# Performance work log

Measured on AMD Instinct MI355X. Metric: run time of the kernel, lower is better.

## Reference

```python
import jax, jax.numpy as jnp
import numpy as np

B, L, D_MODEL = 2, 1024, 512
N_LAYERS, D_STATE, D_CONV = 6, 16, 4
D_INNER = 2 * D_MODEL          # Mamba default expand=2
DT_RANK = (D_MODEL + 15) // 16  # ceil(d_model/16) = 32
EPS = 1.1920929e-07             # torch RMSNorm default eps (fp32 machine eps)


def rmsnorm(x, w):
    return x * jax.lax.rsqrt(jnp.mean(x * x, axis=-1, keepdims=True) + EPS) * w


def selective_scan(u, dt, A, Bm, Cm, Dv):
    # u, dt: (B,L,E); A: (E,N); Bm, Cm: (B,L,N); Dv: (E,)
    dA = jnp.exp(jnp.einsum('ble,en->blen', dt, A))    # discretized A (ZOH)
    dBu = jnp.einsum('ble,bln->blen', dt * u, Bm)      # discretized B * u (Euler)

    def step(h, inp):
        dA_t, dBu_t, C_t = inp
        h = dA_t * h + dBu_t                           # (B,E,N) state update
        y = jnp.einsum('ben,bn->be', h, C_t)
        return h, y

    h0 = jnp.zeros((u.shape[0], u.shape[2], A.shape[1]), u.dtype)
    _, ys = jax.lax.scan(step, h0,
                         (dA.transpose(1, 0, 2, 3), dBu.transpose(1, 0, 2, 3),
                          Cm.transpose(1, 0, 2)))
    return ys.transpose(1, 0, 2) + u * Dv


def mamba_block(x, p):
    xz = jnp.einsum('bld,ed->ble', x, p['in_proj_w'])  # (B,L,2E)
    xi, z = jnp.split(xz, 2, axis=-1)
    # causal depthwise conv1d (kernel D_CONV) + bias + SiLU
    xc = jnp.pad(xi.transpose(0, 2, 1), ((0, 0), (0, 0), (D_CONV - 1, 0)))
    xc = jax.lax.conv_general_dilated(xc, p['conv_w'][:, None, :], (1,), 'VALID',
                                      feature_group_count=D_INNER)
    xi = jax.nn.silu(xc.transpose(0, 2, 1) + p['conv_b'])
    dbc = jnp.einsum('ble,re->blr', xi, p['x_proj_w'])  # (B,L,R+2N)
    dt, Bm, Cm = jnp.split(dbc, [DT_RANK, DT_RANK + D_STATE], axis=-1)
    dt = jax.nn.softplus(jnp.einsum('blr,er->ble', dt, p['dt_w']) + p['dt_b'])
    y = selective_scan(xi, dt, -jnp.exp(p['A_log']), Bm, Cm, p['D'])
    y = y * jax.nn.silu(z)                              # gate branch
    return jnp.einsum('ble,de->bld', y, p['out_w'])


def setup_inputs() -> dict:
    key = jax.random.key(0)
    ks = jax.random.split(key, 8)
    s = 0.02
    return {
        'x': jax.random.normal(ks[0], (B, L, D_MODEL), jnp.float32),
        'position_embedding': jax.random.normal(ks[1], (B, L, D_MODEL), jnp.float32) * 0.02,
        'norm_w': jnp.ones((D_MODEL,), jnp.float32),
        'in_proj_w': jax.random.normal(ks[2], (N_LAYERS, 2 * D_INNER, D_MODEL), jnp.float32) * s,
        'conv_w': jax.random.normal(ks[3], (N_LAYERS, D_INNER, D_CONV), jnp.float32) * 0.2,
        'conv_b': jnp.zeros((N_LAYERS, D_INNER), jnp.float32),
        'x_proj_w': jax.random.normal(ks[4], (N_LAYERS, DT_RANK + 2 * D_STATE, D_INNER), jnp.float32) * s,
        'dt_w': jax.random.normal(ks[5], (N_LAYERS, D_INNER, DT_RANK), jnp.float32) * s,
        'dt_b': jnp.full((N_LAYERS, D_INNER), -4.6, jnp.float32),  # softplus(dt_b) ~ 0.01
        'A_log': jnp.broadcast_to(
            jnp.log(jnp.arange(1, D_STATE + 1, dtype=jnp.float32)),
            (N_LAYERS, D_INNER, D_STATE)) + jnp.zeros((N_LAYERS, D_INNER, D_STATE), jnp.float32),
        'D': jnp.ones((N_LAYERS, D_INNER), jnp.float32),
        'out_w': jax.random.normal(ks[6], (N_LAYERS, D_MODEL, D_INNER), jnp.float32) * s,
    }


def reference(x, position_embedding, norm_w, in_proj_w, conv_w, conv_b,
              x_proj_w, dt_w, dt_b, A_log, D, out_w):
    stacked = dict(in_proj_w=in_proj_w, conv_w=conv_w, conv_b=conv_b,
                   x_proj_w=x_proj_w, dt_w=dt_w, dt_b=dt_b,
                   A_log=A_log, D=D, out_w=out_w)

    def body(h, p):
        h = h + position_embedding          # added at the start of every layer
        h = mamba_block(rmsnorm(h, norm_w), p)  # NOTE: no residual, per source
        return h, None

    h, _ = jax.lax.scan(body, x, stacked)
    return h
```

## Files before the change

kernel.cpp:

```cpp
#include <hip/hip_runtime.h>
#include <hip/hip_bf16.h>


typedef __attribute__((ext_vector_type(8))) short bf16x8;
typedef __attribute__((ext_vector_type(4))) float f32x4;

__device__ __forceinline__ float bf2f(unsigned short u) {
    unsigned int x = ((unsigned int)u) << 16;
    return __builtin_bit_cast(float, x);
}
__device__ __forceinline__ unsigned short f2bf(float f) {
    __hip_bfloat16 h = __float2bfloat16(f);
    return __builtin_bit_cast(unsigned short, h);
}
__device__ __forceinline__ float ldin(const void* p, size_t i, int isbf) {
    return isbf ? bf2f(((const unsigned short*)p)[i]) : ((const float*)p)[i];
}
__device__ __forceinline__ float softplus_f(float x) {
    return (x > 20.f) ? x : log1pf(__expf(x));
}
__device__ __forceinline__ void split2(float x, unsigned short& h, unsigned short& l) {
    h = f2bf(x);
    l = f2bf(x - bf2f(h));
}

#define S1 (6*2048*512)
#define S2 (6*512*1024)
#define S3 (6*64*1024)
#define S4 (6*1024*32)
__global__ __launch_bounds__(256) void wsplit_all(
    const void* __restrict__ ipw, const void* __restrict__ ow,
    const void* __restrict__ xpw, const void* __restrict__ dtw,
    const void* __restrict__ Dw,
    unsigned short* __restrict__ h1, unsigned short* __restrict__ l1,
    unsigned short* __restrict__ h2, unsigned short* __restrict__ l2,
    unsigned short* __restrict__ h3, unsigned short* __restrict__ l3,
    unsigned short* __restrict__ h4, unsigned short* __restrict__ l4,
    int* __restrict__ flag)
{
    int g = blockIdx.x * 256 + threadIdx.x;
    const int isbf = (*(const unsigned int*)Dw == 0x3F800000u) ? 0 : 1;
    if (g == 0) *flag = isbf;
    const void* src; unsigned short *dh, *dl; int i;
    if (g < S1)                { src = ipw; dh = h1; dl = l1; i = g; }
    else if (g < S1+S2)        { src = ow;  dh = h2; dl = l2; i = g - S1; }
    else if (g < S1+S2+S3)     { src = xpw; dh = h3; dl = l3; i = g - S1 - S2; }
    else if (g < S1+S2+S3+S4)  { src = dtw; dh = h4; dl = l4; i = g - S1 - S2 - S3; }
    else return;
    unsigned short hh, ll;
    split2(ldin(src, i, isbf), hh, ll);
    dh[i] = hh; dl[i] = ll;
}

__global__ __launch_bounds__(256) void gemm128(
    const unsigned short* __restrict__ Ah, const unsigned short* __restrict__ Al,
    int lda,
    const unsigned short* __restrict__ Wh, const unsigned short* __restrict__ Wl,
    long woff,
    float* __restrict__ Cf, int N, int K)
{
    __shared__ __align__(16) unsigned short As[2][128][40];
    __shared__ __align__(16) unsigned short Ws[2][128][40];

    const int m0 = blockIdx.x * 128, n0 = blockIdx.y * 128;
    const int t = threadIdx.x, lane = t & 63, wave = t >> 6;
    const int wm = (wave & 1) * 64, wn = (wave >> 1) * 64;
    const int srow = t >> 1, scol = (t & 1) * 16;

    const unsigned short* ah = Ah + (size_t)(m0 + srow) * lda + scol;
    const unsigned short* al = Al + (size_t)(m0 + srow) * lda + scol;
    const unsigned short* wh = Wh + woff + (size_t)(n0 + srow) * K + scol;
    const unsigned short* wl = Wl + woff + (size_t)(n0 + srow) * K + scol;

    f32x4 acc[4][4] = {};
    const int fm = lane & 15, fk = (lane >> 4) * 8;

    for (int k0 = 0; k0 < K; k0 += 32) {
        __syncthreads();
        *(uint4*)(&As[0][srow][scol])     = *(const uint4*)(ah + k0);
        *(uint4*)(&As[0][srow][scol + 8]) = *(const uint4*)(ah + k0 + 8);
        *(uint4*)(&As[1][srow][scol])     = *(const uint4*)(al + k0);
        *(uint4*)(&As[1][srow][scol + 8]) = *(const uint4*)(al + k0 + 8);
        *(uint4*)(&Ws[0][srow][scol])     = *(const uint4*)(wh + k0);
        *(uint4*)(&Ws[0][srow][scol + 8]) = *(const uint4*)(wh + k0 + 8);
        *(uint4*)(&Ws[1][srow][scol])     = *(const uint4*)(wl + k0);
        *(uint4*)(&Ws[1][srow][scol + 8]) = *(const uint4*)(wl + k0 + 8);
        __syncthreads();

        bf16x8 a_h[4], a_l[4], w_h[4], w_l[4];
#pragma unroll
        for (int i = 0; i < 4; ++i) {
            a_h[i] = *(const bf16x8*)(&As[0][wm + i * 16 + fm][fk]);
            a_l[i] = *(const bf16x8*)(&As[1][wm + i * 16 + fm][fk]);
            w_h[i] = *(const bf16x8*)(&Ws[0][wn + i * 16 + fm][fk]);
            w_l[i] = *(const bf16x8*)(&Ws[1][wn + i * 16 + fm][fk]);
        }
#pragma unroll
        for (int mi = 0; mi < 4; ++mi)
#pragma unroll
            for (int ni = 0; ni < 4; ++ni) {
                acc[mi][ni] = __builtin_amdgcn_mfma_f32_16x16x32_bf16(
                    a_h[mi], w_h[ni], acc[mi][ni], 0, 0, 0);
                acc[mi][ni] = __builtin_amdgcn_mfma_f32_16x16x32_bf16(
                    a_h[mi], w_l[ni], acc[mi][ni], 0, 0, 0);
                acc[mi][ni] = __builtin_amdgcn_mfma_f32_16x16x32_bf16(
                    a_l[mi], w_h[ni], acc[mi][ni], 0, 0, 0);
            }
    }

    const int col = lane & 15, rb = (lane >> 4) * 4;
#pragma unroll
    for (int mi = 0; mi < 4; ++mi)
#pragma unroll
        for (int ni = 0; ni < 4; ++ni)
#pragma unroll
            for (int r = 0; r < 4; ++r) {
                int gm = m0 + wm + mi * 16 + rb + r;
                int gn = n0 + wn + ni * 16 + col;
                Cf[(size_t)gm * N + gn] = acc[mi][ni][r];
            }
}

template <int ACT>
__global__ __launch_bounds__(256) void gemm_hl(
    const unsigned short* __restrict__ Ah, const unsigned short* __restrict__ Al,
    int lda,
    const unsigned short* __restrict__ Wh, const unsigned short* __restrict__ Wl,
    long woff,
    float* __restrict__ Cf, long zstride,
    const void* __restrict__ bias, long boff, const int* __restrict__ flag,
    int N, int K, int Kc)
{
    const int isbf = *flag;
    __shared__ __align__(16) unsigned short As[2][64][40];
    __shared__ __align__(16) unsigned short Ws[2][64][40];

    const int m0 = blockIdx.x * 64, n0 = blockIdx.y * 64;
    const int kb = blockIdx.z * Kc;
    const int t = threadIdx.x;
    const int lane = t & 63, wave = t >> 6;
    const int wm = (wave & 1) * 32, wn = (wave >> 1) * 32;
    const int srow = t >> 2, scol = (t & 3) * 8;

    const unsigned short* ah = Ah + (size_t)(m0 + srow) * lda + scol;
    const unsigned short* al = Al + (size_t)(m0 + srow) * lda + scol;
    const unsigned short* wh = Wh + woff + (size_t)(n0 + srow) * K + scol;
    const unsigned short* wl = Wl + woff + (size_t)(n0 + srow) * K + scol;

    f32x4 acc[2][2] = {};

    for (int k0 = kb; k0 < kb + Kc; k0 += 32) {
        __syncthreads();
        *(uint4*)(&As[0][srow][scol]) = *(const uint4*)(ah + k0);
        *(uint4*)(&As[1][srow][scol]) = *(const uint4*)(al + k0);
        *(uint4*)(&Ws[0][srow][scol]) = *(const uint4*)(wh + k0);
        *(uint4*)(&Ws[1][srow][scol]) = *(const uint4*)(wl + k0);
        __syncthreads();

        const int fm = lane & 15, fk = (lane >> 4) * 8;
        bf16x8 a0h = *(const bf16x8*)(&As[0][wm + fm][fk]);
        bf16x8 a1h = *(const bf16x8*)(&As[0][wm + 16 + fm][fk]);
        bf16x8 w0h = *(const bf16x8*)(&Ws[0][wn + fm][fk]);
        bf16x8 w1h = *(const bf16x8*)(&Ws[0][wn + 16 + fm][fk]);
        bf16x8 a0l = *(const bf16x8*)(&As[1][wm + fm][fk]);
        bf16x8 a1l = *(const bf16x8*)(&As[1][wm + 16 + fm][fk]);
        bf16x8 w0l = *(const bf16x8*)(&Ws[1][wn + fm][fk]);
        bf16x8 w1l = *(const bf16x8*)(&Ws[1][wn + 16 + fm][fk]);

        acc[0][0] = __builtin_amdgcn_mfma_f32_16x16x32_bf16(a0h, w0h, acc[0][0], 0, 0, 0);
        acc[0][1] = __builtin_amdgcn_mfma_f32_16x16x32_bf16(a0h, w1h, acc[0][1], 0, 0, 0);
        acc[1][0] = __builtin_amdgcn_mfma_f32_16x16x32_bf16(a1h, w0h, acc[1][0], 0, 0, 0);
        acc[1][1] = __builtin_amdgcn_mfma_f32_16x16x32_bf16(a1h, w1h, acc[1][1], 0, 0, 0);
        acc[0][0] = __builtin_amdgcn_mfma_f32_16x16x32_bf16(a0h, w0l, acc[0][0], 0, 0, 0);
        acc[0][1] = __builtin_amdgcn_mfma_f32_16x16x32_bf16(a0h, w1l, acc[0][1], 0, 0, 0);
        acc[1][0] = __builtin_amdgcn_mfma_f32_16x16x32_bf16(a1h, w0l, acc[1][0], 0, 0, 0);
        acc[1][1] = __builtin_amdgcn_mfma_f32_16x16x32_bf16(a1h, w1l, acc[1][1], 0, 0, 0);
        acc[0][0] = __builtin_amdgcn_mfma_f32_16x16x32_bf16(a0l, w0h, acc[0][0], 0, 0, 0);
        acc[0][1] = __builtin_amdgcn_mfma_f32_16x16x32_bf16(a0l, w1h, acc[0][1], 0, 0, 0);
        acc[1][0] = __builtin_amdgcn_mfma_f32_16x16x32_bf16(a1l, w0h, acc[1][0], 0, 0, 0);
        acc[1][1] = __builtin_amdgcn_mfma_f32_16x16x32_bf16(a1l, w1h, acc[1][1], 0, 0, 0);
    }

    float* Cp = Cf + (size_t)blockIdx.z * zstride;
    const int col = lane & 15, rb = (lane >> 4) * 4;
#pragma unroll
    for (int mi = 0; mi < 2; ++mi)
#pragma unroll
        for (int ni = 0; ni < 2; ++ni)
#pragma unroll
            for (int r = 0; r < 4; ++r) {
                int gm = m0 + wm + mi * 16 + rb + r;
                int gn = n0 + wn + ni * 16 + col;
                float v = acc[mi][ni][r];
                if (bias) v += ldin(bias, boff + gn, isbf);
                if (ACT == 1) v = softplus_f(v);
                Cp[(size_t)gm * N + gn] = v;
            }
}

__global__ __launch_bounds__(256) void xp_reduce(
    const float* __restrict__ Pxp, float* __restrict__ dbc,
    unsigned short* __restrict__ dth, unsigned short* __restrict__ dtl)
{
    int g = blockIdx.x * 256 + threadIdx.x;
    float s = 0.f;
#pragma unroll
    for (int z = 0; z < 8; ++z) s += Pxp[(size_t)z * 131072 + g];
    dbc[g] = s;
    int n = g & 63, t = g >> 6;
    if (n < 32) {
        unsigned short hh, ll;
        split2(s, hh, ll);
        dth[t * 32 + n] = hh; dtl[t * 32 + n] = ll;
    }
}

__global__ __launch_bounds__(256) void rmsnorm_k(
    const void* __restrict__ hsrc, int hdyn, const void* __restrict__ pos,
    const void* __restrict__ nw, const int* __restrict__ flag,
    unsigned short* __restrict__ xnh, unsigned short* __restrict__ xnl)
{
    const int isbf = *flag;
    const int row = blockIdx.x;
    const int t = threadIdx.x;
    const size_t base = (size_t)row * 512;
    float h0 = hdyn ? ldin(hsrc, base + t, isbf)       : ((const float*)hsrc)[base + t];
    float h1 = hdyn ? ldin(hsrc, base + 256 + t, isbf) : ((const float*)hsrc)[base + 256 + t];
    float v0 = h0 + ldin(pos, base + t, isbf);
    float v1 = h1 + ldin(pos, base + 256 + t, isbf);
    float ss = v0 * v0 + v1 * v1;
#pragma unroll
    for (int o = 32; o; o >>= 1) ss += __shfl_xor(ss, o, 64);
    __shared__ float sw[4];
    if ((t & 63) == 0) sw[t >> 6] = ss;
    __syncthreads();
    float tot = sw[0] + sw[1] + sw[2] + sw[3];
    float sc = rsqrtf(tot * (1.0f / 512.0f) + 1.1920929e-07f);
    float o0 = v0 * sc * ldin(nw, t, isbf);
    float o1 = v1 * sc * ldin(nw, 256 + t, isbf);
    unsigned short hh, ll;
    split2(o0, hh, ll); xnh[base + t] = hh;       xnl[base + t] = ll;
    split2(o1, hh, ll); xnh[base + 256 + t] = hh; xnl[base + 256 + t] = ll;
}

__global__ __launch_bounds__(256) void conv_silu_k(
    const float* __restrict__ xz,
    const void* __restrict__ cw, long cwoff,
    const void* __restrict__ cb, long cboff,
    const int* __restrict__ flag,
    float* __restrict__ xi,
    unsigned short* __restrict__ xih, unsigned short* __restrict__ xil)
{
    const int isbf = *flag;
    int g = blockIdx.x * 256 + threadIdx.x;
    int e = g & 1023;
    int l = (g >> 10) & 1023;
    int b = g >> 20;
    float acc = ldin(cb, cboff + e, isbf);
#pragma unroll
    for (int k = 0; k < 4; ++k) {
        int ls = l - 3 + k;
        if (ls >= 0)
            acc += ldin(cw, cwoff + e * 4 + k, isbf) *
                   xz[((size_t)(b * 1024 + ls)) * 2048 + e];
    }
    acc = acc / (1.f + __expf(-acc));
    xi[g] = acc;
    unsigned short hh, ll;
    split2(acc, hh, ll);
    xih[g] = hh; xil[g] = ll;
}

#define CL 16
#define NCH 64

__global__ __launch_bounds__(256) void scan_stage1(
    const float* __restrict__ dtp, const float* __restrict__ u,
    const float* __restrict__ dbc,
    const void* __restrict__ alog, long aoff, const int* __restrict__ flag,
    float* __restrict__ P, float* __restrict__ S)
{
    const int isbf = *flag;
    int g = blockIdx.x * 256 + threadIdx.x;
    int e = g & 1023, c = (g >> 10) & (NCH - 1), b = g >> 16;
    int t0 = b * 1024 + c * CL;

    float dv[CL], uv[CL];
#pragma unroll
    for (int i = 0; i < CL; ++i) {
        dv[i] = dtp[(size_t)(t0 + i) * 1024 + e];
        uv[i] = u[(size_t)(t0 + i) * 1024 + e];
    }

    float Aen[16], Pn[16], Sn[16];
#pragma unroll
    for (int n = 0; n < 16; ++n) {
        Aen[n] = -__expf(ldin(alog, aoff + e * 16 + n, isbf));
        Pn[n] = 1.f; Sn[n] = 0.f;
    }
#pragma unroll
    for (int i = 0; i < CL; ++i) {
        float d = dv[i], du = d * uv[i];
        const float4* Bp = (const float4*)(dbc + (size_t)(t0 + i) * 64 + 32);
        float4 b0 = Bp[0], b1 = Bp[1], b2 = Bp[2], b3 = Bp[3];
        float Bt[16] = {b0.x,b0.y,b0.z,b0.w, b1.x,b1.y,b1.z,b1.w,
                        b2.x,b2.y,b2.z,b2.w, b3.x,b3.y,b3.z,b3.w};
#pragma unroll
        for (int n = 0; n < 16; ++n) {
            float a = __expf(d * Aen[n]);
            Sn[n] = a * Sn[n] + du * Bt[n];
            Pn[n] *= a;
        }
    }
    size_t ob = ((size_t)(b * NCH + c) * 16) * 1024 + e;
#pragma unroll
    for (int n = 0; n < 16; ++n) {
        P[ob + (size_t)n * 1024] = Pn[n];
        S[ob + (size_t)n * 1024] = Sn[n];
    }
}

__global__ __launch_bounds__(256) void scan_stage2(
    float* __restrict__ PH, const float* __restrict__ S)
{
    int g = blockIdx.x * 256 + threadIdx.x;
    int e = g & 1023, n = (g >> 10) & 15, b = g >> 14;
    float H = 0.f;
    for (int cb = 0; cb < NCH; cb += 8) {
        float p[8], s[8];
#pragma unroll
        for (int j = 0; j < 8; ++j) {
            size_t idx = ((size_t)(b * NCH + cb + j) * 16 + n) * 1024 + e;
            p[j] = PH[idx]; s[j] = S[idx];
        }
#pragma unroll
        for (int j = 0; j < 8; ++j) {
            size_t idx = ((size_t)(b * NCH + cb + j) * 16 + n) * 1024 + e;
            PH[idx] = H;
            H = p[j] * H + s[j];
        }
    }
}

__global__ __launch_bounds__(256) void scan_stage3(
    const float* __restrict__ dtp, const float* __restrict__ u,
    const float* __restrict__ dbc,
    const void* __restrict__ alog, long aoff,
    const void* __restrict__ Dv, long doff,
    const int* __restrict__ flag,
    const float* __restrict__ xz, const float* __restrict__ H0,
    unsigned short* __restrict__ yh, unsigned short* __restrict__ yl)
{
    const int isbf = *flag;
    int g = blockIdx.x * 256 + threadIdx.x;
    int e = g & 1023, c = (g >> 10) & (NCH - 1), b = g >> 16;
    int t0 = b * 1024 + c * CL;

    float dv[CL], uv[CL], zv[CL];
#pragma unroll
    for (int i = 0; i < CL; ++i) {
        dv[i] = dtp[(size_t)(t0 + i) * 1024 + e];
        uv[i] = u[(size_t)(t0 + i) * 1024 + e];
        zv[i] = xz[(size_t)(t0 + i) * 2048 + 1024 + e];
    }

    float Aen[16], h[16];
    size_t ob = ((size_t)(b * NCH + c) * 16) * 1024 + e;
#pragma unroll
    for (int n = 0; n < 16; ++n) {
        Aen[n] = -__expf(ldin(alog, aoff + e * 16 + n, isbf));
        h[n] = H0[ob + (size_t)n * 1024];
    }
    float De = ldin(Dv, doff + e, isbf);
#pragma unroll
    for (int i = 0; i < CL; ++i) {
        float d = dv[i], uu = uv[i], du = d * uu;
        const float4* Bp = (const float4*)(dbc + (size_t)(t0 + i) * 64 + 32);
        float4 b0 = Bp[0], b1 = Bp[1], b2 = Bp[2], b3 = Bp[3];
        float4 c0 = Bp[4], c1 = Bp[5], c2 = Bp[6], c3 = Bp[7];
        float Bt[16] = {b0.x,b0.y,b0.z,b0.w, b1.x,b1.y,b1.z,b1.w,
                        b2.x,b2.y,b2.z,b2.w, b3.x,b3.y,b3.z,b3.w};
        float Ct[16] = {c0.x,c0.y,c0.z,c0.w, c1.x,c1.y,c1.z,c1.w,
                        c2.x,c2.y,c2.z,c2.w, c3.x,c3.y,c3.z,c3.w};
        float y = 0.f;
#pragma unroll
        for (int n = 0; n < 16; ++n) {
            float a = __expf(d * Aen[n]);
            h[n] = a * h[n] + du * Bt[n];
            y += h[n] * Ct[n];
        }
        float sz = zv[i] / (1.f + __expf(-zv[i]));
        float yv = (y + uu * De) * sz;
        unsigned short hh, ll;
        split2(yv, hh, ll);
        yh[(size_t)(t0 + i) * 1024 + e] = hh;
        yl[(size_t)(t0 + i) * 1024 + e] = ll;
    }
}

extern "C" void kernel_launch(void* const* d_in, const int* in_sizes, int n_in,
                              void* d_out, int out_size, void* d_ws, size_t ws_size,
                              hipStream_t stream)
{
    const void* x    = d_in[0];
    const void* pos  = d_in[1];
    const void* nw   = d_in[2];
    const void* ipw  = d_in[3];
    const void* cw   = d_in[4];
    const void* cb   = d_in[5];
    const void* xpw  = d_in[6];
    const void* dtw  = d_in[7];
    const void* dtb  = d_in[8];
    const void* alog = d_in[9];
    const void* Dw   = d_in[10];
    const void* ow   = d_in[11];

    char* w = (char*)d_ws;
    auto take = [&](size_t bytes) { char* p = w; w += (bytes + 255) & ~255ull; return p; };

    float* h    = (float*)take(2048ull * 512 * 4);
    float* xz   = (float*)take(2048ull * 2048 * 4);
    float* xi   = (float*)take(2048ull * 1024 * 4);
    float* dtf  = (float*)take(2048ull * 1024 * 4);
    float* dbc  = (float*)take(2048ull * 64 * 4);
    float* P    = (float*)take(2ull * NCH * 16 * 1024 * 4);
    float* S    = (float*)take(2ull * NCH * 16 * 1024 * 4);
    float* Pxp  = (float*)take(8ull * 2048 * 64 * 4);
    unsigned short* xnh = (unsigned short*)take(2048ull * 512 * 2);
    unsigned short* xnl = (unsigned short*)take(2048ull * 512 * 2);
    unsigned short* xih = (unsigned short*)take(2048ull * 1024 * 2);
    unsigned short* xil = (unsigned short*)take(2048ull * 1024 * 2);
    unsigned short* yh  = (unsigned short*)take(2048ull * 1024 * 2);
    unsigned short* yl  = (unsigned short*)take(2048ull * 1024 * 2);
    unsigned short* dth = (unsigned short*)take(2048ull * 32 * 2);
    unsigned short* dtl = (unsigned short*)take(2048ull * 32 * 2);
    unsigned short* wip_h = (unsigned short*)take(6ull * 2048 * 512 * 2);
    unsigned short* wip_l = (unsigned short*)take(6ull * 2048 * 512 * 2);
    unsigned short* wow_h = (unsigned short*)take(6ull * 512 * 1024 * 2);
    unsigned short* wow_l = (unsigned short*)take(6ull * 512 * 1024 * 2);
    unsigned short* wxp_h = (unsigned short*)take(6ull * 64 * 1024 * 2);
    unsigned short* wxp_l = (unsigned short*)take(6ull * 64 * 1024 * 2);
    unsigned short* wdt_h = (unsigned short*)take(6ull * 1024 * 32 * 2);
    unsigned short* wdt_l = (unsigned short*)take(6ull * 1024 * 32 * 2);
    int* flag = (int*)take(256);

    wsplit_all<<<(S1 + S2 + S3 + S4 + 255) / 256, 256, 0, stream>>>(
        ipw, ow, xpw, dtw, Dw,
        wip_h, wip_l, wow_h, wow_l, wxp_h, wxp_l, wdt_h, wdt_l, flag);

    for (int l = 0; l < 6; ++l) {
        rmsnorm_k<<<2048, 256, 0, stream>>>(
            l == 0 ? x : (const void*)h, l == 0 ? 1 : 0, pos, nw, flag, xnh, xnl);
        gemm128<<<dim3(16, 16), 256, 0, stream>>>(
            xnh, xnl, 512, wip_h, wip_l, (long)l * 2048 * 512, xz, 2048, 512);
        conv_silu_k<<<8192, 256, 0, stream>>>(xz, cw, (long)l * 4096, cb, (long)l * 1024,
                                              flag, xi, xih, xil);
        gemm_hl<0><<<dim3(32, 1, 8), 256, 0, stream>>>(
            xih, xil, 1024, wxp_h, wxp_l, (long)l * 64 * 1024,
            Pxp, 2048l * 64, nullptr, 0, flag, 64, 1024, 128);
        xp_reduce<<<512, 256, 0, stream>>>(Pxp, dbc, dth, dtl);
        gemm_hl<1><<<dim3(32, 16), 256, 0, stream>>>(
            dth, dtl, 32, wdt_h, wdt_l, (long)l * 1024 * 32,
            dtf, 0, dtb, (long)l * 1024, flag, 1024, 32, 32);
        scan_stage1<<<512, 256, 0, stream>>>(dtf, xi, dbc, alog, (long)l * 16384,
                                             flag, P, S);
        scan_stage2<<<128, 256, 0, stream>>>(P, S);
        scan_stage3<<<512, 256, 0, stream>>>(dtf, xi, dbc, alog, (long)l * 16384,
                                             Dw, (long)l * 1024, flag, xz, P, yh, yl);
        float* outp = (l < 5) ? h : (float*)d_out;
        gemm_hl<0><<<dim3(32, 8), 256, 0, stream>>>(
            yh, yl, 1024, wow_h, wow_l, (long)l * 512 * 1024,
            outp, 0, nullptr, 0, flag, 512, 1024, 1024);
    }
}
```

Measured before the change: 860.1 us.

## Fuse dt projection and softplus into scan kernels, fold z-gate SiLU into in_proj GEMM

The separate dt_proj GEMM and its dt buffer are removed. Each scan thread now computes its dt from the 32 low-rank values in dbc and its own row of dt_w, then applies softplus, in both stage1 and stage3. The in_proj GEMM is retiled to 128x64 and splits its output: x goes to a compact fp32 buffer and SiLU(z) is stored as bf16. The scans read u back from the hi/lo bf16 pair instead of an fp32 copy. This cuts kernel launches and memory traffic, at the cost of recomputing the dt dot product in two scan stages and a slight loss of precision on the gate.

```diff
diff --git a/kernel.cpp b/kernel.cpp
--- a/kernel.cpp
+++ b/kernel.cpp
@@ -27,78 +27,75 @@
 #define S1 (6*2048*512)
 #define S2 (6*512*1024)
 #define S3 (6*64*1024)
-#define S4 (6*1024*32)
 __global__ __launch_bounds__(256) void wsplit_all(
     const void* __restrict__ ipw, const void* __restrict__ ow,
-    const void* __restrict__ xpw, const void* __restrict__ dtw,
-    const void* __restrict__ Dw,
+    const void* __restrict__ xpw, const void* __restrict__ Dw,
     unsigned short* __restrict__ h1, unsigned short* __restrict__ l1,
     unsigned short* __restrict__ h2, unsigned short* __restrict__ l2,
     unsigned short* __restrict__ h3, unsigned short* __restrict__ l3,
-    unsigned short* __restrict__ h4, unsigned short* __restrict__ l4,
     int* __restrict__ flag)
 {
     int g = blockIdx.x * 256 + threadIdx.x;
     const int isbf = (*(const unsigned int*)Dw == 0x3F800000u) ? 0 : 1;
     if (g == 0) *flag = isbf;
     const void* src; unsigned short *dh, *dl; int i;
-    if (g < S1)                { src = ipw; dh = h1; dl = l1; i = g; }
-    else if (g < S1+S2)        { src = ow;  dh = h2; dl = l2; i = g - S1; }
-    else if (g < S1+S2+S3)     { src = xpw; dh = h3; dl = l3; i = g - S1 - S2; }
-    else if (g < S1+S2+S3+S4)  { src = dtw; dh = h4; dl = l4; i = g - S1 - S2 - S3; }
+    if (g < S1)             { src = ipw; dh = h1; dl = l1; i = g; }
+    else if (g < S1+S2)     { src = ow;  dh = h2; dl = l2; i = g - S1; }
+    else if (g < S1+S2+S3)  { src = xpw; dh = h3; dl = l3; i = g - S1 - S2; }
     else return;
     unsigned short hh, ll;
     split2(ldin(src, i, isbf), hh, ll);
     dh[i] = hh; dl[i] = ll;
 }
 
-__global__ __launch_bounds__(256) void gemm128(
+__global__ __launch_bounds__(256) void gemm_in(
     const unsigned short* __restrict__ Ah, const unsigned short* __restrict__ Al,
-    int lda,
     const unsigned short* __restrict__ Wh, const unsigned short* __restrict__ Wl,
     long woff,
-    float* __restrict__ Cf, int N, int K)
+    float* __restrict__ xf, unsigned short* __restrict__ zg)
 {
     __shared__ __align__(16) unsigned short As[2][128][40];
-    __shared__ __align__(16) unsigned short Ws[2][128][40];
-
-    const int m0 = blockIdx.x * 128, n0 = blockIdx.y * 128;
+    __shared__ __align__(16) unsigned short Ws[2][64][40];
+
+    const int m0 = blockIdx.x * 128, n0 = blockIdx.y * 64;
     const int t = threadIdx.x, lane = t & 63, wave = t >> 6;
-    const int wm = (wave & 1) * 64, wn = (wave >> 1) * 64;
-    const int srow = t >> 1, scol = (t & 1) * 16;
-
-    const unsigned short* ah = Ah + (size_t)(m0 + srow) * lda + scol;
-    const unsigned short* al = Al + (size_t)(m0 + srow) * lda + scol;
-    const unsigned short* wh = Wh + woff + (size_t)(n0 + srow) * K + scol;
-    const unsigned short* wl = Wl + woff + (size_t)(n0 + srow) * K + scol;
-
-    f32x4 acc[4][4] = {};
+    const int wm = (wave & 1) * 64, wn = (wave >> 1) * 32;
+    const int sra = t >> 1, sca = (t & 1) * 16;
+    const int srw = t >> 2, scw = (t & 3) * 8;
+
+    const unsigned short* ah = Ah + (size_t)(m0 + sra) * 512 + sca;
+    const unsigned short* al = Al + (size_t)(m0 + sra) * 512 + sca;
+    const unsigned short* wh = Wh + woff + (size_t)(n0 + srw) * 512 + scw;
+    const unsigned short* wl = Wl + woff + (size_t)(n0 + srw) * 512 + scw;
+
+    f32x4 acc[4][2] = {};
     const int fm = lane & 15, fk = (lane >> 4) * 8;
 
-    for (int k0 = 0; k0 < K; k0 += 32) {
+    for (int k0 = 0; k0 < 512; k0 += 32) {
         __syncthreads();
-        *(uint4*)(&As[0][srow][scol])     = *(const uint4*)(ah + k0);
-        *(uint4*)(&As[0][srow][scol + 8]) = *(const uint4*)(ah + k0 + 8);
-        *(uint4*)(&As[1][srow][scol])     = *(const uint4*)(al + k0);
-        *(uint4*)(&As[1][srow][scol + 8]) = *(const uint4*)(al + k0 + 8);
-        *(uint4*)(&Ws[0][srow][scol])     = *(const uint4*)(wh + k0);
-        *(uint4*)(&Ws[0][srow][scol + 8]) = *(const uint4*)(wh + k0 + 8);
-        *(uint4*)(&Ws[1][srow][scol])     = *(const uint4*)(wl + k0);
-        *(uint4*)(&Ws[1][srow][scol + 8]) = *(const uint4*)(wl + k0 + 8);
+        *(uint4*)(&As[0][sra][sca])     = *(const uint4*)(ah + k0);
+        *(uint4*)(&As[0][sra][sca + 8]) = *(const uint4*)(ah + k0 + 8);
+        *(uint4*)(&As[1][sra][sca])     = *(const uint4*)(al + k0);
+        *(uint4*)(&As[1][sra][sca + 8]) = *(const uint4*)(al + k0 + 8);
+        *(uint4*)(&Ws[0][srw][scw])     = *(const uint4*)(wh + k0);
+        *(uint4*)(&Ws[1][srw][scw])     = *(const uint4*)(wl + k0);
         __syncthreads();
 
-        bf16x8 a_h[4], a_l[4], w_h[4], w_l[4];
+        bf16x8 a_h[4], a_l[4], w_h[2], w_l[2];
 #pragma unroll
         for (int i = 0; i < 4; ++i) {
             a_h[i] = *(const bf16x8*)(&As[0][wm + i * 16 + fm][fk]);
             a_l[i] = *(const bf16x8*)(&As[1][wm + i * 16 + fm][fk]);
+        }
+#pragma unroll
+        for (int i = 0; i < 2; ++i) {
             w_h[i] = *(const bf16x8*)(&Ws[0][wn + i * 16 + fm][fk]);
             w_l[i] = *(const bf16x8*)(&Ws[1][wn + i * 16 + fm][fk]);
         }
 #pragma unroll
         for (int mi = 0; mi < 4; ++mi)
 #pragma unroll
-            for (int ni = 0; ni < 4; ++ni) {
+            for (int ni = 0; ni < 2; ++ni) {
                 acc[mi][ni] = __builtin_amdgcn_mfma_f32_16x16x32_bf16(
                     a_h[mi], w_h[ni], acc[mi][ni], 0, 0, 0);
                 acc[mi][ni] = __builtin_amdgcn_mfma_f32_16x16x32_bf16(
@@ -109,29 +106,33 @@
     }
 
     const int col = lane & 15, rb = (lane >> 4) * 4;
+    const int zhalf = (n0 >= 1024);
 #pragma unroll
     for (int mi = 0; mi < 4; ++mi)
 #pragma unroll
-        for (int ni = 0; ni < 4; ++ni)
+        for (int ni = 0; ni < 2; ++ni)
 #pragma unroll
             for (int r = 0; r < 4; ++r) {
                 int gm = m0 + wm + mi * 16 + rb + r;
                 int gn = n0 + wn + ni * 16 + col;
-                Cf[(size_t)gm * N + gn] = acc[mi][ni][r];
+                float v = acc[mi][ni][r];
+                if (!zhalf) {
+                    xf[(size_t)gm * 1024 + gn] = v;
+                } else {
+                    float sv = v / (1.f + __expf(-v));
+                    zg[(size_t)gm * 1024 + (gn - 1024)] = f2bf(sv);
+                }
             }
 }
 
-template <int ACT>
 __global__ __launch_bounds__(256) void gemm_hl(
     const unsigned short* __restrict__ Ah, const unsigned short* __restrict__ Al,
     int lda,
     const unsigned short* __restrict__ Wh, const unsigned short* __restrict__ Wl,
     long woff,
     float* __restrict__ Cf, long zstride,
-    const void* __restrict__ bias, long boff, const int* __restrict__ flag,
     int N, int K, int Kc)
 {
-    const int isbf = *flag;
     __shared__ __align__(16) unsigned short As[2][64][40];
     __shared__ __align__(16) unsigned short Ws[2][64][40];
 
@@ -191,28 +192,18 @@
             for (int r = 0; r < 4; ++r) {
                 int gm = m0 + wm + mi * 16 + rb + r;
                 int gn = n0 + wn + ni * 16 + col;
-                float v = acc[mi][ni][r];
-                if (bias) v += ldin(bias, boff + gn, isbf);
-                if (ACT == 1) v = softplus_f(v);
-                Cp[(size_t)gm * N + gn] = v;
+                Cp[(size_t)gm * N + gn] = acc[mi][ni][r];
             }
 }
 
 __global__ __launch_bounds__(256) void xp_reduce(
-    const float* __restrict__ Pxp, float* __restrict__ dbc,
-    unsigned short* __restrict__ dth, unsigned short* __restrict__ dtl)
+    const float* __restrict__ Pxp, float* __restrict__ dbc)
 {
     int g = blockIdx.x * 256 + threadIdx.x;
     float s = 0.f;
 #pragma unroll
     for (int z = 0; z < 8; ++z) s += Pxp[(size_t)z * 131072 + g];
     dbc[g] = s;
-    int n = g & 63, t = g >> 6;
-    if (n < 32) {
-        unsigned short hh, ll;
-        split2(s, hh, ll);
-        dth[t * 32 + n] = hh; dtl[t * 32 + n] = ll;
-    }
 }
 
 __global__ __launch_bounds__(256) void rmsnorm_k(
@@ -244,11 +235,10 @@
 }
 
 __global__ __launch_bounds__(256) void conv_silu_k(
-    const float* __restrict__ xz,
+    const float* __restrict__ xf,
     const void* __restrict__ cw, long cwoff,
     const void* __restrict__ cb, long cboff,
     const int* __restrict__ flag,
-    float* __restrict__ xi,
     unsigned short* __restrict__ xih, unsigned short* __restrict__ xil)
 {
     const int isbf = *flag;
@@ -262,10 +252,9 @@
         int ls = l - 3 + k;
         if (ls >= 0)
             acc += ldin(cw, cwoff + e * 4 + k, isbf) *
-                   xz[((size_t)(b * 1024 + ls)) * 2048 + e];
+                   xf[((size_t)(b * 1024 + ls)) * 1024 + e];
     }
     acc = acc / (1.f + __expf(-acc));
-    xi[g] = acc;
     unsigned short hh, ll;
     split2(acc, hh, ll);
     xih[g] = hh; xil[g] = ll;
@@ -275,8 +264,10 @@
 #define NCH 64
 
 __global__ __launch_bounds__(256) void scan_stage1(
-    const float* __restrict__ dtp, const float* __restrict__ u,
+    const unsigned short* __restrict__ xih, const unsigned short* __restrict__ xil,
     const float* __restrict__ dbc,
+    const void* __restrict__ dtw, long dtwoff,
+    const void* __restrict__ dtb, long dtboff,
     const void* __restrict__ alog, long aoff, const int* __restrict__ flag,
     float* __restrict__ P, float* __restrict__ S)
 {
@@ -285,12 +276,16 @@
     int e = g & 1023, c = (g >> 10) & (NCH - 1), b = g >> 16;
     int t0 = b * 1024 + c * CL;
 
-    float dv[CL], uv[CL];
+    float uv[CL];
 #pragma unroll
     for (int i = 0; i < CL; ++i) {
-        dv[i] = dtp[(size_t)(t0 + i) * 1024 + e];
-        uv[i] = u[(size_t)(t0 + i) * 1024 + e];
-    }
+        size_t ix = (size_t)(t0 + i) * 1024 + e;
+        uv[i] = bf2f(xih[ix]) + bf2f(xil[ix]);
+    }
+    float wr[32];
+#pragma unroll
+    for (int r = 0; r < 32; ++r) wr[r] = ldin(dtw, dtwoff + (size_t)e * 32 + r, isbf);
+    float dbias = ldin(dtb, dtboff + e, isbf);
 
     float Aen[16], Pn[16], Sn[16];
 #pragma unroll
@@ -300,9 +295,16 @@
     }
 #pragma unroll
     for (int i = 0; i < CL; ++i) {
-        float d = dv[i], du = d * uv[i];
-        const float4* Bp = (const float4*)(dbc + (size_t)(t0 + i) * 64 + 32);
-        float4 b0 = Bp[0], b1 = Bp[1], b2 = Bp[2], b3 = Bp[3];
+        const float4* Rp = (const float4*)(dbc + (size_t)(t0 + i) * 64);
+        float dtv = dbias;
+#pragma unroll
+        for (int q = 0; q < 8; ++q) {
+            float4 rq = Rp[q];
+            dtv += rq.x * wr[q*4] + rq.y * wr[q*4+1] + rq.z * wr[q*4+2] + rq.w * wr[q*4+3];
+        }
+        float d = softplus_f(dtv);
+        float du = d * uv[i];
+        float4 b0 = Rp[8], b1 = Rp[9], b2 = Rp[10], b3 = Rp[11];
         float Bt[16] = {b0.x,b0.y,b0.z,b0.w, b1.x,b1.y,b1.z,b1.w,
                         b2.x,b2.y,b2.z,b2.w, b3.x,b3.y,b3.z,b3.w};
 #pragma unroll
@@ -343,12 +345,14 @@
 }
 
 __global__ __launch_bounds__(256) void scan_stage3(
-    const float* __restrict__ dtp, const float* __restrict__ u,
+    const unsigned short* __restrict__ xih, const unsigned short* __restrict__ xil,
     const float* __restrict__ dbc,
+    const void* __restrict__ dtw, long dtwoff,
+    const void* __restrict__ dtb, long dtboff,
     const void* __restrict__ alog, long aoff,
     const void* __restrict__ Dv, long doff,
     const int* __restrict__ flag,
-    const float* __restrict__ xz, const float* __restrict__ H0,
+    const unsigned short* __restrict__ zg, const float* __restrict__ H0,
     unsigned short* __restrict__ yh, unsigned short* __restrict__ yl)
 {
     const int isbf = *flag;
@@ -356,13 +360,17 @@
     int e = g & 1023, c = (g >> 10) & (NCH - 1), b = g >> 16;
     int t0 = b * 1024 + c * CL;
 
-    float dv[CL], uv[CL], zv[CL];
+    float uv[CL], gv[CL];
 #pragma unroll
     for (int i = 0; i < CL; ++i) {
-        dv[i] = dtp[(size_t)(t0 + i) * 1024 + e];
-        uv[i] = u[(size_t)(t0 + i) * 1024 + e];
-        zv[i] = xz[(size_t)(t0 + i) * 2048 + 1024 + e];
-    }
+        size_t ix = (size_t)(t0 + i) * 1024 + e;
+        uv[i] = bf2f(xih[ix]) + bf2f(xil[ix]);
+        gv[i] = bf2f(zg[ix]);
+    }
+    float wr[32];
+#pragma unroll
+    for (int r = 0; r < 32; ++r) wr[r] = ldin(dtw, dtwoff + (size_t)e * 32 + r, isbf);
+    float dbias = ldin(dtb, dtboff + e, isbf);
 
     float Aen[16], h[16];
     size_t ob = ((size_t)(b * NCH + c) * 16) * 1024 + e;
@@ -374,10 +382,18 @@
     float De = ldin(Dv, doff + e, isbf);
 #pragma unroll
     for (int i = 0; i < CL; ++i) {
-        float d = dv[i], uu = uv[i], du = d * uu;
-        const float4* Bp = (const float4*)(dbc + (size_t)(t0 + i) * 64 + 32);
-        float4 b0 = Bp[0], b1 = Bp[1], b2 = Bp[2], b3 = Bp[3];
-        float4 c0 = Bp[4], c1 = Bp[5], c2 = Bp[6], c3 = Bp[7];
+        const float4* Rp = (const float4*)(dbc + (size_t)(t0 + i) * 64);
+        float dtv = dbias;
+#pragma unroll
+        for (int q = 0; q < 8; ++q) {
+            float4 rq = Rp[q];
+            dtv += rq.x * wr[q*4] + rq.y * wr[q*4+1] + rq.z * wr[q*4+2] + rq.w * wr[q*4+3];
+        }
+        float d = softplus_f(dtv);
+        float uu = uv[i];
+        float du = d * uu;
+        float4 b0 = Rp[8],  b1 = Rp[9],  b2 = Rp[10], b3 = Rp[11];
+        float4 c0 = Rp[12], c1 = Rp[13], c2 = Rp[14], c3 = Rp[15];
         float Bt[16] = {b0.x,b0.y,b0.z,b0.w, b1.x,b1.y,b1.z,b1.w,
                         b2.x,b2.y,b2.z,b2.w, b3.x,b3.y,b3.z,b3.w};
         float Ct[16] = {c0.x,c0.y,c0.z,c0.w, c1.x,c1.y,c1.z,c1.w,
@@ -389,8 +405,7 @@
             h[n] = a * h[n] + du * Bt[n];
             y += h[n] * Ct[n];
         }
-        float sz = zv[i] / (1.f + __expf(-zv[i]));
-        float yv = (y + uu * De) * sz;
+        float yv = (y + uu * De) * gv[i];
         unsigned short hh, ll;
         split2(yv, hh, ll);
         yh[(size_t)(t0 + i) * 1024 + e] = hh;
@@ -419,9 +434,8 @@
     auto take = [&](size_t bytes) { char* p = w; w += (bytes + 255) & ~255ull; return p; };
 
     float* h    = (float*)take(2048ull * 512 * 4);
-    float* xz   = (float*)take(2048ull * 2048 * 4);
-    float* xi   = (float*)take(2048ull * 1024 * 4);
-    float* dtf  = (float*)take(2048ull * 1024 * 4);
+    float* xf   = (float*)take(2048ull * 1024 * 4);
+    unsigned short* zg = (unsigned short*)take(2048ull * 1024 * 2);
     float* dbc  = (float*)take(2048ull * 64 * 4);
     float* P    = (float*)take(2ull * NCH * 16 * 1024 * 4);
     float* S    = (float*)take(2ull * NCH * 16 * 1024 * 4);
@@ -432,44 +446,39 @@
     unsigned short* xil = (unsigned short*)take(2048ull * 1024 * 2);
     unsigned short* yh  = (unsigned short*)take(2048ull * 1024 * 2);
     unsigned short* yl  = (unsigned short*)take(2048ull * 1024 * 2);
-    unsigned short* dth = (unsigned short*)take(2048ull * 32 * 2);
-    unsigned short* dtl = (unsigned short*)take(2048ull * 32 * 2);
     unsigned short* wip_h = (unsigned short*)take(6ull * 2048 * 512 * 2);
     unsigned short* wip_l = (unsigned short*)take(6ull * 2048 * 512 * 2);
     unsigned short* wow_h = (unsigned short*)take(6ull * 512 * 1024 * 2);
     unsigned short* wow_l = (unsigned short*)take(6ull * 512 * 1024 * 2);
     unsigned short* wxp_h = (unsigned short*)take(6ull * 64 * 1024 * 2);
     unsigned short* wxp_l = (unsigned short*)take(6ull * 64 * 1024 * 2);
-    unsigned short* wdt_h = (unsigned short*)take(6ull * 1024 * 32 * 2);
-    unsigned short* wdt_l = (unsigned short*)take(6ull * 1024 * 32 * 2);
     int* flag = (int*)take(256);
 
-    wsplit_all<<<(S1 + S2 + S3 + S4 + 255) / 256, 256, 0, stream>>>(
-        ipw, ow, xpw, dtw, Dw,
-        wip_h, wip_l, wow_h, wow_l, wxp_h, wxp_l, wdt_h, wdt_l, flag);
+    wsplit_all<<<(S1 + S2 + S3 + 255) / 256, 256, 0, stream>>>(
+        ipw, ow, xpw, Dw,
+        wip_h, wip_l, wow_h, wow_l, wxp_h, wxp_l, flag);
 
     for (int l = 0; l < 6; ++l) {
         rmsnorm_k<<<2048, 256, 0, stream>>>(
             l == 0 ? x : (const void*)h, l == 0 ? 1 : 0, pos, nw, flag, xnh, xnl);
-        gemm128<<<dim3(16, 16), 256, 0, stream>>>(
-            xnh, xnl, 512, wip_h, wip_l, (long)l * 2048 * 512, xz, 2048, 512);
-        conv_silu_k<<<8192, 256, 0, stream>>>(xz, cw, (long)l * 4096, cb, (long)l * 1024,
-                                              flag, xi, xih, xil);
-        gemm_hl<0><<<dim3(32, 1, 8), 256, 0, stream>>>(
+        gemm_in<<<dim3(16, 32), 256, 0, stream>>>(
+            xnh, xnl, wip_h, wip_l, (long)l * 2048 * 512, xf, zg);
+        conv_silu_k<<<8192, 256, 0, stream>>>(xf, cw, (long)l * 4096, cb, (long)l * 1024,
+                                              flag, xih, xil);
+        gemm_hl<<<dim3(32, 1, 8), 256, 0, stream>>>(
             xih, xil, 1024, wxp_h, wxp_l, (long)l * 64 * 1024,
-            Pxp, 2048l * 64, nullptr, 0, flag, 64, 1024, 128);
-        xp_reduce<<<512, 256, 0, stream>>>(Pxp, dbc, dth, dtl);
-        gemm_hl<1><<<dim3(32, 16), 256, 0, stream>>>(
-            dth, dtl, 32, wdt_h, wdt_l, (long)l * 1024 * 32,
-            dtf, 0, dtb, (long)l * 1024, flag, 1024, 32, 32);
-        scan_stage1<<<512, 256, 0, stream>>>(dtf, xi, dbc, alog, (long)l * 16384,
-                                             flag, P, S);
+            Pxp, 2048l * 64, 64, 1024, 128);
+        xp_reduce<<<512, 256, 0, stream>>>(Pxp, dbc);
+        scan_stage1<<<512, 256, 0, stream>>>(
+            xih, xil, dbc, dtw, (long)l * 1024 * 32, dtb, (long)l * 1024,
+            alog, (long)l * 16384, flag, P, S);
         scan_stage2<<<128, 256, 0, stream>>>(P, S);
-        scan_stage3<<<512, 256, 0, stream>>>(dtf, xi, dbc, alog, (long)l * 16384,
-                                             Dw, (long)l * 1024, flag, xz, P, yh, yl);
+        scan_stage3<<<512, 256, 0, stream>>>(
+            xih, xil, dbc, dtw, (long)l * 1024 * 32, dtb, (long)l * 1024,
+            alog, (long)l * 16384, Dw, (long)l * 1024, flag, zg, P, yh, yl);
         float* outp = (l < 5) ? h : (float*)d_out;
-        gemm_hl<0><<<dim3(32, 8), 256, 0, stream>>>(
+        gemm_hl<<<dim3(32, 8), 256, 0, stream>>>(
             yh, yl, 1024, wow_h, wow_l, (long)l * 512 * 1024,
-            outp, 0, nullptr, 0, flag, 512, 1024, 1024);
-    }
-}
+            outp, 0, 512, 1024, 1024);
+    }
+}
```

Result: slower. 1.114 ms (+29.6%).
